# Kernel optimization log

Hardware: AMD Instinct MI355X
Metric: run time of the kernel (lower is better)

## Reference

```python
import jax, jax.numpy as jnp
import numpy as np

NUM_EXPERTS = 8
HIDDEN = 1024
INTER = 1024
BATCH = 2
SEQ = 1024
TOP_K = 2
SWIGLU_ALPHA = 1.702
LIMIT = 7.0


def setup_inputs() -> dict:
    key = jax.random.key(0)
    ks = jax.random.split(key, 7)
    hidden_states = jax.random.normal(ks[0], (BATCH, SEQ, HIDDEN), jnp.float32)
    router_indices = jax.random.randint(ks[1], (BATCH * SEQ, TOP_K), 0, NUM_EXPERTS)
    routing_weights = jax.nn.softmax(
        jax.random.normal(ks[2], (BATCH * SEQ, NUM_EXPERTS), jnp.float32), axis=-1)
    scale = 0.02
    gate_up_proj = jax.random.normal(ks[3], (NUM_EXPERTS, HIDDEN, 2 * INTER), jnp.float32) * scale
    gate_up_proj_bias = jax.random.normal(ks[4], (NUM_EXPERTS, 2 * INTER), jnp.float32) * scale
    down_proj = jax.random.normal(ks[5], (NUM_EXPERTS, INTER, HIDDEN), jnp.float32) * scale
    down_proj_bias = jax.random.normal(ks[6], (NUM_EXPERTS, HIDDEN), jnp.float32) * scale
    return {
        "hidden_states": hidden_states,
        "router_indices": router_indices,
        "routing_weights": routing_weights,
        "gate_up_proj": gate_up_proj,
        "gate_up_proj_bias": gate_up_proj_bias,
        "down_proj": down_proj,
        "down_proj_bias": down_proj_bias,
    }


def _grouped_mm(x, w, expert_ids):
    """Grouped GEMM: y[t] = x[t] @ w[expert_ids[t]].

    x: [T, K], w: [E, K, N], expert_ids: [T] int.
    Reference form via one-hot masking (exact equivalent of torch._grouped_mm
    on expert-sorted tokens); guaranteed jit- and grad-safe.
    """
    onehot = jax.nn.one_hot(expert_ids, w.shape[0], dtype=x.dtype)  # [T, E]
    y_all = jnp.einsum('tk,ekn->etn', x, w)                         # [E, T, N]
    return jnp.einsum('te,etn->tn', onehot, y_all)                  # [T, N]


def _gpt_oss_swiglu(x):
    gate = jnp.minimum(x[..., ::2], LIMIT)
    up = jnp.clip(x[..., 1::2], -LIMIT, LIMIT)
    glu = gate * jax.nn.sigmoid(gate * SWIGLU_ALPHA)
    return (up + 1.0) * glu


def reference(hidden_states, router_indices, routing_weights,
              gate_up_proj, gate_up_proj_bias, down_proj, down_proj_bias):
    B = hidden_states.shape[0]
    H = hidden_states.shape[-1]
    x = hidden_states.reshape(-1, H)                       # [M, H]
    M = x.shape[0]
    top_k = router_indices.shape[1]
    num_experts = gate_up_proj.shape[0]

    # routing_weights is [M, num_experts] -> gather the top-k weights
    topk_weights = jnp.take_along_axis(routing_weights, router_indices, axis=1)  # [M, K]

    flat_experts = router_indices.reshape(-1)              # [T = M*K]
    sort_idx = jnp.argsort(flat_experts)                   # expert-sorted order
    sorted_pos = sort_idx // top_k                         # token id per slot
    expert_sorted = flat_experts[sort_idx]                 # [T]
    grouped = x[sorted_pos]                                # [T, H]

    gate_up = _grouped_mm(grouped, gate_up_proj, expert_sorted)
    gate_up = gate_up + gate_up_proj_bias[expert_sorted]   # per-expert bias
    inter = _gpt_oss_swiglu(gate_up)                       # [T, I]

    down = _grouped_mm(inter, down_proj, expert_sorted)
    down = down + down_proj_bias[expert_sorted]            # [T, H]
    down = down * topk_weights.reshape(-1)[sort_idx][:, None]

    out = jnp.zeros((M, H), x.dtype).at[sorted_pos].add(down)  # scatter-add combine
    return out.reshape(B, -1, H)
```

## Files before the change

kernel.cpp:

```cpp
#include <hip/hip_runtime.h>

#define NE 8
#define NH 1024
#define NI 1024
#define NGU 2048
#define MTOK 2048
#define TSLOT 4096

#define MAXT64 80
#define MAXT128 40

typedef short s16x8 __attribute__((ext_vector_type(8)));
typedef float f32x4 __attribute__((ext_vector_type(4)));
typedef unsigned short u16;

#define WS_SEG      0
#define WS_DESC64   64
#define WS_DESC128  384
#define WS_SLOT     1024
#define WS_POS      17408
#define WS_INTER    33792
#define WS_AREG     8422400UL
#define WS_WREG     12616704UL
#define WS_WTD      46171136UL
#define WS_NEED_FAST  46171136UL
#define WS_NEED_PIGGY 62948352UL

__device__ inline u16 f2bf(float f) {
    unsigned u = __builtin_bit_cast(unsigned, f);
    u += 0x7fffu + ((u >> 16) & 1u);
    return (u16)(u >> 16);
}

__device__ inline void lds_dma16(const u16* g, u16* l) {
    __builtin_amdgcn_global_load_lds(
        (const __attribute__((address_space(1))) unsigned int*)g,
        (__attribute__((address_space(3))) unsigned int*)l, 16, 0, 0);
}

__device__ inline int lds_off(int row, int blk) {
    return (row << 7) | (((blk ^ (row & 7)) & 7) << 4);
}

#define PIPE_FENCE asm volatile("" ::: "memory")
#define WAIT_VM6   asm volatile("s_waitcnt vmcnt(6)" ::: "memory")
#define WAIT_VM0   asm volatile("s_waitcnt vmcnt(0)" ::: "memory")

__device__ inline void tr_tile(const float* __restrict__ in, u16* __restrict__ outw,
                               int K, int N, int n0, int k0, int tid, u16 (*T)[66]) {
#pragma unroll
    for (int p = 0; p < 2; ++p) {
        int kr = p * 32 + (tid >> 4) * 2;
        int nc = (tid & 15) * 4;
        const float* r0 = in + (size_t)(k0 + kr) * N + n0 + nc;
        float4 v0 = *(const float4*)r0;
        float4 v1 = *(const float4*)(r0 + N);
#pragma unroll
        for (int i = 0; i < 4; ++i) {
            unsigned lo = f2bf(((const float*)&v0)[i]);
            unsigned hi = f2bf(((const float*)&v1)[i]);
            *(unsigned*)&T[nc + i][kr] = lo | (hi << 16);
        }
    }
    __syncthreads();
#pragma unroll
    for (int p = 0; p < 2; ++p) {
        int idx = p * 256 + tid;
        int nr = idx >> 3, kc = (idx & 7) * 8;
        unsigned q0 = *(const unsigned*)&T[nr][kc + 0];
        unsigned q1 = *(const unsigned*)&T[nr][kc + 2];
        unsigned q2 = *(const unsigned*)&T[nr][kc + 4];
        unsigned q3 = *(const unsigned*)&T[nr][kc + 6];
        uint4 vv = {q0, q1, q2, q3};
        *(uint4*)(outw + (size_t)(n0 + nr) * K + k0 + kc) = vv;
    }
}

__device__ inline void build_body(const int* __restrict__ ridx, int* __restrict__ seg,
                                  int* __restrict__ d64, int* __restrict__ d128,
                                  int* __restrict__ slot_of, int* __restrict__ pos_of,
                                  int* cnt, int* cur, int tid) {
    if (tid < NE) cnt[tid] = 0;
    __syncthreads();
    for (int s = tid; s < TSLOT; s += 256) atomicAdd(&cnt[ridx[s] & 7], 1);
    __syncthreads();
    if (tid == 0) {
        int a = 0;
        for (int e = 0; e < NE; ++e) { seg[e] = a; cur[e] = a; a += cnt[e]; }
        seg[NE] = a;
        int nt = 0;
        for (int e = 0; e < NE; ++e)
            for (int m0 = 0; m0 < cnt[e]; m0 += 64) d64[nt++] = (e << 16) | (m0 / 64);
        for (; nt < MAXT64; ++nt) d64[nt] = -1;
        nt = 0;
        for (int e = 0; e < NE; ++e)
            for (int m0 = 0; m0 < cnt[e]; m0 += 128) d128[nt++] = (e << 16) | (m0 / 128);
        for (; nt < MAXT128; ++nt) d128[nt] = -1;
    }
    __syncthreads();
    for (int s = tid; s < TSLOT; s += 256) {
        int e = ridx[s] & 7;
        int p = atomicAdd(&cur[e], 1);
        slot_of[p] = s;
        pos_of[s] = p;
    }
}

__device__ __forceinline__ void gemm_pipe(const u16* const ap[4], const u16* const bp[2],
                                          char* SM, int tid, int kbeg, int nsteps,
                                          f32x4 (&acc)[4][2]) {
    u16* As0 = (u16*)SM;
    u16* As1 = (u16*)(SM + 16384);
    u16* Bs0 = (u16*)(SM + 32768);
    u16* Bs1 = (u16*)(SM + 40960);
    int lane = tid & 63, w = tid >> 6;
    int ml = lane & 15, kq = lane >> 4;
    int wm = w >> 1, wn = w & 1;

    auto stage = [&](u16* AS, u16* BS, int kb) {
#pragma unroll
        for (int c = 0; c < 4; ++c) lds_dma16(ap[c] + kb, AS + c * 2048 + w * 512);
#pragma unroll
        for (int c = 0; c < 2; ++c) lds_dma16(bp[c] + kb, BS + c * 2048 + w * 512);
    };
    auto compute = [&](const u16* AS, const u16* BS) {
#pragma unroll
        for (int kk = 0; kk < 64; kk += 32) {
            s16x8 af[4], bf[2];
#pragma unroll
            for (int i = 0; i < 4; ++i)
                af[i] = *(const s16x8*)((const char*)AS + lds_off(wm * 64 + i * 16 + ml, (kk >> 3) + kq));
#pragma unroll
            for (int i = 0; i < 2; ++i)
                bf[i] = *(const s16x8*)((const char*)BS + lds_off(wn * 32 + i * 16 + ml, (kk >> 3) + kq));
#pragma unroll
            for (int mi = 0; mi < 4; ++mi)
#pragma unroll
                for (int ni = 0; ni < 2; ++ni)
                    acc[mi][ni] = __builtin_amdgcn_mfma_f32_16x16x32_bf16(
                        af[mi], bf[ni], acc[mi][ni], 0, 0, 0);
        }
    };

    stage(As0, Bs0, kbeg);
    for (int t = 0; t < nsteps; t += 2) {
        stage(As1, Bs1, kbeg + ((t + 1) << 6));
        WAIT_VM6;
        __builtin_amdgcn_s_barrier();
        PIPE_FENCE;
        __builtin_amdgcn_s_setprio(1);
        compute(As0, Bs0);
        __builtin_amdgcn_s_setprio(0);
        PIPE_FENCE;
        __builtin_amdgcn_s_barrier();
        if (t < nsteps - 2) {
            stage(As0, Bs0, kbeg + ((t + 2) << 6));
            WAIT_VM6;
        } else {
            WAIT_VM0;
        }
        __builtin_amdgcn_s_barrier();
        PIPE_FENCE;
        __builtin_amdgcn_s_setprio(1);
        compute(As1, Bs1);
        __builtin_amdgcn_s_setprio(0);
        PIPE_FENCE;
        __builtin_amdgcn_s_barrier();
    }
}

__device__ __forceinline__ void job_gateup(
        int d, int y, const u16* __restrict__ A, const u16* __restrict__ wt,
        const float* __restrict__ bias, const int* __restrict__ seg,
        const int* __restrict__ slot_of, u16* __restrict__ inter,
        char* SM, int tid) {
    int e = d >> 16, mt = d & 0xffff;
    int seg0 = seg[e], Te = seg[e + 1] - seg0, m0 = mt * 128;
    int lane = tid & 63, w = tid >> 6;
    int ml = lane & 15, kq = lane >> 4;
    int wm = w >> 1, wn = w & 1;
    int n0 = y * 64;
    int dr = lane >> 3, db = (lane & 7) ^ dr;
    const u16* wte = wt + (size_t)e * NGU * NH;

    const u16* ap[4];
#pragma unroll
    for (int c = 0; c < 4; ++c) {
        int gr = seg0 + m0 + c * 32 + w * 8 + dr;
        if (gr > TSLOT - 1) gr = TSLOT - 1;
        int tok = slot_of[gr] >> 1;
        ap[c] = A + (size_t)tok * NH + db * 8;
    }
    const u16* bp[2];
#pragma unroll
    for (int c = 0; c < 2; ++c)
        bp[c] = wte + (size_t)(n0 + c * 32 + w * 8 + dr) * NH + db * 8;

    f32x4 zero = {0.f, 0.f, 0.f, 0.f};
    f32x4 acc[4][2];
#pragma unroll
    for (int i = 0; i < 4; ++i) { acc[i][0] = zero; acc[i][1] = zero; }

    gemm_pipe(ap, bp, SM, tid, 0, 16, acc);

#pragma unroll
    for (int ni = 0; ni < 2; ++ni) {
        int n = n0 + wn * 32 + ni * 16 + ml;
        float bv = bias[e * NGU + n];
#pragma unroll
        for (int mi = 0; mi < 4; ++mi) {
#pragma unroll
            for (int r = 0; r < 4; ++r) {
                float v = acc[mi][ni][r] + bv;
                float pr = __shfl_xor(v, 1, 64);
                float g = (lane & 1) ? pr : v;
                float u = (lane & 1) ? v : pr;
                g = fminf(g, 7.0f);
                u = fminf(fmaxf(u, -7.0f), 7.0f);
                float glu = g / (1.0f + __expf(-1.702f * g));
                float yv = (u + 1.0f) * glu;
                int mloc = wm * 64 + mi * 16 + kq * 4 + r;
                if (!(lane & 1) && (m0 + mloc) < Te)
                    inter[(size_t)(seg0 + m0 + mloc) * NI + (n >> 1)] = f2bf(yv);
            }
        }
    }
}

__device__ __forceinline__ void job_down(
        int d, int y, int kz, const u16* __restrict__ inter, const u16* __restrict__ wt,
        const float* __restrict__ bias, const float* __restrict__ rw,
        const int* __restrict__ seg, const int* __restrict__ slot_of,
        float* __restrict__ out, char* SM, int tid) {
    int e = d >> 16, mt = d & 0xffff;
    int seg0 = seg[e], Te = seg[e + 1] - seg0, m0 = mt * 128;
    int* tokS = (int*)(SM + 49152);
    float* wgtS = (float*)(SM + 49664);

    if (tid < 128) {
        int m = m0 + tid;
        if (m < Te) {
            int token = slot_of[seg0 + m] >> 1;
            tokS[tid] = token;
            wgtS[tid] = rw[token * NE + e];
        } else {
            tokS[tid] = 0;
            wgtS[tid] = 0.0f;
        }
    }

    int lane = tid & 63, w = tid >> 6;
    int ml = lane & 15, kq = lane >> 4;
    int wm = w >> 1, wn = w & 1;
    int n0 = y * 64;
    int dr = lane >> 3, db = (lane & 7) ^ dr;
    const u16* wte = wt + (size_t)e * NH * NI;

    const u16* ap[4];
#pragma unroll
    for (int c = 0; c < 4; ++c) {
        int gr = seg0 + m0 + c * 32 + w * 8 + dr;
        if (gr > TSLOT - 1) gr = TSLOT - 1;
        ap[c] = inter + (size_t)gr * NI + db * 8;
    }
    const u16* bp[2];
#pragma unroll
    for (int c = 0; c < 2; ++c)
        bp[c] = wte + (size_t)(n0 + c * 32 + w * 8 + dr) * NI + db * 8;

    f32x4 zero = {0.f, 0.f, 0.f, 0.f};
    f32x4 acc[4][2];
#pragma unroll
    for (int i = 0; i < 4; ++i) { acc[i][0] = zero; acc[i][1] = zero; }

    gemm_pipe(ap, bp, SM, tid, kz * (NI / 2), 8, acc);

    float bv[2];
#pragma unroll
    for (int ni = 0; ni < 2; ++ni)
        bv[ni] = kz ? 0.0f : bias[e * NH + n0 + wn * 32 + ni * 16 + ml];

#pragma unroll
    for (int mi = 0; mi < 4; ++mi) {
#pragma unroll
        for (int r = 0; r < 4; ++r) {
            int mloc = wm * 64 + mi * 16 + kq * 4 + r;
            if ((m0 + mloc) < Te) {
                int token = tokS[mloc];
                float wgt = wgtS[mloc];
#pragma unroll
                for (int ni = 0; ni < 2; ++ni) {
                    int n = n0 + wn * 32 + ni * 16 + ml;
                    atomicAdd(&out[(size_t)token * NH + n], (acc[mi][ni][r] + bv[ni]) * wgt);
                }
            }
        }
    }
}

__global__ __launch_bounds__(256) void k_prep(
        const float* __restrict__ x, const int* __restrict__ ridx,
        const float* __restrict__ wgu, const float* __restrict__ wd,
        int* __restrict__ seg, int* __restrict__ d64, int* __restrict__ d128,
        int* __restrict__ slot_of, int* __restrict__ pos_of,
        u16* __restrict__ A, u16* __restrict__ wt_gu, u16* __restrict__ wt_d,
        float* __restrict__ out) {
    __shared__ int cnt[NE];
    __shared__ int cur[NE];
    __shared__ u16 T[64][66];
    int b = blockIdx.x;
    int tid = threadIdx.x;
    if (b == 0) {
        build_body(ridx, seg, d64, d128, slot_of, pos_of, cnt, cur, tid);
    } else if (b <= MTOK) {
        int t = b - 1;
        float4 v = ((const float4*)(x + (size_t)t * NH))[tid];
        ushort4 o;
        o.x = f2bf(v.x); o.y = f2bf(v.y); o.z = f2bf(v.z); o.w = f2bf(v.w);
        ((ushort4*)(A + (size_t)t * NH))[tid] = o;
        float4 z = {0.f, 0.f, 0.f, 0.f};
        ((float4*)(out + (size_t)t * NH))[tid] = z;
    } else if (b <= MTOK + 4096) {
        int id = b - (MTOK + 1);
        int e = id >> 9, rem = id & 511;
        int kblk = rem >> 5, nblk = rem & 31;
        tr_tile(wgu + (size_t)e * NH * NGU, wt_gu + (size_t)e * NGU * NH,
                NH, NGU, nblk * 64, kblk * 64, tid, T);
    } else {
        int id = b - (MTOK + 4097);
        int e = id >> 8, rem = id & 255;
        int kblk = rem >> 4, nblk = rem & 15;
        tr_tile(wd + (size_t)e * NI * NH, wt_d + (size_t)e * NH * NI,
                NI, NH, nblk * 64, kblk * 64, tid, T);
    }
}

__global__ __launch_bounds__(256) void k_gateup_f(
        const u16* __restrict__ A, const u16* __restrict__ wt,
        const float* __restrict__ bias,
        const int* __restrict__ seg, const int* __restrict__ desc,
        const int* __restrict__ slot_of, u16* __restrict__ inter) {
    __shared__ __align__(16) char SM[50176];
    int d = desc[blockIdx.x];
    if (d < 0) return;
    job_gateup(d, blockIdx.y, A, wt, bias, seg, slot_of, inter, SM, threadIdx.x);
}

__global__ __launch_bounds__(256) void k_down_f(
        const u16* __restrict__ inter, const u16* __restrict__ wt,
        const float* __restrict__ bias, const float* __restrict__ rw,
        const int* __restrict__ seg, const int* __restrict__ desc,
        const int* __restrict__ slot_of, float* __restrict__ out) {
    __shared__ __align__(16) char SM[50176];
    int d = desc[blockIdx.x];
    if (d < 0) return;
    job_down(d, blockIdx.y, blockIdx.z, inter, wt, bias, rw, seg, slot_of, out,
             SM, threadIdx.x);
}

__global__ __launch_bounds__(256) void k_tr(const float* __restrict__ W,
                                            u16* __restrict__ WT, int K, int N) {
    __shared__ u16 T[64][66];
    tr_tile(W + (size_t)blockIdx.z * K * N, WT + (size_t)blockIdx.z * N * K,
            K, N, blockIdx.x * 64, blockIdx.y * 64, threadIdx.x, T);
}

__global__ void k_build(const int* __restrict__ ridx, int* __restrict__ seg,
                        int* __restrict__ d64, int* __restrict__ d128,
                        int* __restrict__ slot_of, int* __restrict__ pos_of) {
    __shared__ int cnt[NE];
    __shared__ int cur[NE];
    build_body(ridx, seg, d64, d128, slot_of, pos_of, cnt, cur, threadIdx.x);
}

__global__ __launch_bounds__(256) void k_gateup_s(
        const float* __restrict__ x, const float* __restrict__ w,
        const float* __restrict__ bias,
        const int* __restrict__ seg, const int* __restrict__ desc,
        const int* __restrict__ slot_of, u16* __restrict__ inter) {
    int d = desc[blockIdx.x];
    if (d < 0) return;
    int e = d >> 16, mt = d & 0xffff;
    int seg0 = seg[e], Te = seg[e + 1] - seg0, m0 = mt * 64;
    __shared__ u16 As[64 * 40];
    __shared__ int tok[64];
    int tid = threadIdx.x;
    if (tid < 64) {
        int m = m0 + tid;
        tok[tid] = (m < Te) ? (slot_of[seg0 + m] >> 1) : -1;
    }
    __syncthreads();
    int lane = tid & 63, wave = tid >> 6;
    int arow = tid >> 2, acol = (tid & 3) * 8;
    int ta = tok[arow];
    int kq = lane >> 4, ml = lane & 15;
    int nb = blockIdx.y * 128 + wave * 32;
    const float* wp = w + (size_t)e * NH * NGU;
    f32x4 zero = {0.f, 0.f, 0.f, 0.f};
    f32x4 acc[4][2];
#pragma unroll
    for (int i = 0; i < 4; ++i) { acc[i][0] = zero; acc[i][1] = zero; }
    for (int kb = 0; kb < NH; kb += 32) {
        float4 a0 = {0, 0, 0, 0}, a1 = {0, 0, 0, 0};
        if (ta >= 0) {
            const float* xp = x + (size_t)ta * NH + kb + acol;
            a0 = *(const float4*)xp; a1 = *(const float4*)(xp + 4);
        }
        s16x8 av;
        av[0] = (short)f2bf(a0.x); av[1] = (short)f2bf(a0.y);
        av[2] = (short)f2bf(a0.z); av[3] = (short)f2bf(a0.w);
        av[4] = (short)f2bf(a1.x); av[5] = (short)f2bf(a1.y);
        av[6] = (short)f2bf(a1.z); av[7] = (short)f2bf(a1.w);
        __syncthreads();
        *(s16x8*)&As[arow * 40 + acol] = av;
        __syncthreads();
        s16x8 afr[4];
#pragma unroll
        for (int msi = 0; msi < 4; ++msi)
            afr[msi] = *(const s16x8*)&As[(msi * 16 + ml) * 40 + kq * 8];
        s16x8 bfr[2];
#pragma unroll
        for (int s = 0; s < 2; ++s) {
            const float* bp = wp + (size_t)(kb + kq * 8) * NGU + nb + s * 16 + ml;
#pragma unroll
            for (int j = 0; j < 8; ++j) bfr[s][j] = (short)f2bf(bp[(size_t)j * NGU]);
        }
#pragma unroll
        for (int msi = 0; msi < 4; ++msi)
#pragma unroll
            for (int s = 0; s < 2; ++s)
                acc[msi][s] = __builtin_amdgcn_mfma_f32_16x16x32_bf16(
                    afr[msi], bfr[s], acc[msi][s], 0, 0, 0);
    }
#pragma unroll
    for (int s = 0; s < 2; ++s) {
        int n = nb + s * 16 + ml;
        float bv = bias[e * NGU + n];
#pragma unroll
        for (int msi = 0; msi < 4; ++msi) {
#pragma unroll
            for (int r = 0; r < 4; ++r) {
                float v = acc[msi][s][r] + bv;
                float pr = __shfl_xor(v, 1, 64);
                float g = (lane & 1) ? pr : v;
                float u = (lane & 1) ? v : pr;
                g = fminf(g, 7.0f);
                u = fminf(fmaxf(u, -7.0f), 7.0f);
                float glu = g / (1.0f + __expf(-1.702f * g));
                float y = (u + 1.0f) * glu;
                int mrow = m0 + msi * 16 + kq * 4 + r;
                if (!(lane & 1) && mrow < Te)
                    inter[(size_t)(seg0 + mrow) * NI + (n >> 1)] = f2bf(y);
            }
        }
    }
}

__global__ __launch_bounds__(256) void k_down_s(
        const u16* __restrict__ inter, const float* __restrict__ w,
        const float* __restrict__ bias, const float* __restrict__ rw,
        const int* __restrict__ seg, const int* __restrict__ desc,
        const int* __restrict__ slot_of, float* __restrict__ out) {
    int d = desc[blockIdx.x];
    if (d < 0) return;
    int e = d >> 16, mt = d & 0xffff;
    int seg0 = seg[e], Te = seg[e + 1] - seg0, m0 = mt * 64;
    __shared__ u16 As[64 * 40];
    int tid = threadIdx.x;
    int lane = tid & 63, wave = tid >> 6;
    int arow = tid >> 2, acol = (tid & 3) * 8;
    bool avalid = (m0 + arow) < Te;
    int kq = lane >> 4, ml = lane & 15;
    int nb = blockIdx.y * 128 + wave * 32;
    const float* wp = w + (size_t)e * NI * NH;
    f32x4 zero = {0.f, 0.f, 0.f, 0.f};
    f32x4 acc[4][2];
#pragma unroll
    for (int i = 0; i < 4; ++i) { acc[i][0] = zero; acc[i][1] = zero; }
    for (int kb = 0; kb < NI; kb += 32) {
        s16x8 av = {0, 0, 0, 0, 0, 0, 0, 0};
        if (avalid) av = *(const s16x8*)(inter + (size_t)(seg0 + m0 + arow) * NI + kb + acol);
        __syncthreads();
        *(s16x8*)&As[arow * 40 + acol] = av;
        __syncthreads();
        s16x8 afr[4];
#pragma unroll
        for (int msi = 0; msi < 4; ++msi)
            afr[msi] = *(const s16x8*)&As[(msi * 16 + ml) * 40 + kq * 8];
        s16x8 bfr[2];
#pragma unroll
        for (int s = 0; s < 2; ++s) {
            const float* bp = wp + (size_t)(kb + kq * 8) * NH + nb + s * 16 + ml;
#pragma unroll
            for (int j = 0; j < 8; ++j) bfr[s][j] = (short)f2bf(bp[(size_t)j * NH]);
        }
#pragma unroll
        for (int msi = 0; msi < 4; ++msi)
#pragma unroll
            for (int s = 0; s < 2; ++s)
                acc[msi][s] = __builtin_amdgcn_mfma_f32_16x16x32_bf16(
                    afr[msi], bfr[s], acc[msi][s], 0, 0, 0);
    }
    float bv[2];
    bv[0] = bias[e * NH + nb + ml];
    bv[1] = bias[e * NH + nb + 16 + ml];
#pragma unroll
    for (int msi = 0; msi < 4; ++msi) {
#pragma unroll
        for (int r = 0; r < 4; ++r) {
            int mrow = m0 + msi * 16 + kq * 4 + r;
            if (mrow < Te) {
                int slot = slot_of[seg0 + mrow];
                int token = slot >> 1;
                float wgt = rw[token * NE + e];
#pragma unroll
                for (int s = 0; s < 2; ++s) {
                    int n = nb + s * 16 + ml;
                    atomicAdd(&out[(size_t)token * NH + n], (acc[msi][s][r] + bv[s]) * wgt);
                }
            }
        }
    }
}

extern "C" void kernel_launch(void* const* d_in, const int* in_sizes, int n_in,
                              void* d_out, int out_size, void* d_ws, size_t ws_size,
                              hipStream_t stream) {
    const float* x   = (const float*)d_in[0];
    const int*   ri  = (const int*)d_in[1];
    const float* rw  = (const float*)d_in[2];
    const float* wgu = (const float*)d_in[3];
    const float* bgu = (const float*)d_in[4];
    const float* wd  = (const float*)d_in[5];
    const float* bd  = (const float*)d_in[6];
    float* out = (float*)d_out;

    char* ws = (char*)d_ws;
    int* seg     = (int*)(ws + WS_SEG);
    int* d64     = (int*)(ws + WS_DESC64);
    int* d128    = (int*)(ws + WS_DESC128);
    int* slot_of = (int*)(ws + WS_SLOT);
    int* pos_of  = (int*)(ws + WS_POS);
    u16* inter   = (u16*)(ws + WS_INTER);

    if (ws_size >= WS_NEED_PIGGY) {
        u16* aReg = (u16*)(ws + WS_AREG);
        u16* wReg = (u16*)(ws + WS_WREG);
        u16* wtd  = (u16*)(ws + WS_WTD);
        hipLaunchKernelGGL(k_prep, dim3(1 + MTOK + 4096 + 2048), dim3(256), 0, stream,
                           x, ri, wgu, wd, seg, d64, d128, slot_of, pos_of,
                           aReg, wReg, wtd, out);
        hipLaunchKernelGGL(k_gateup_f, dim3(MAXT128, NGU / 64), dim3(256), 0, stream,
                           aReg, wReg, bgu, seg, d128, slot_of, inter);
        hipLaunchKernelGGL(k_down_f, dim3(MAXT128, NH / 64, 2), dim3(256), 0, stream,
                           inter, wtd, bd, rw, seg, d128, slot_of, out);
    } else if (ws_size >= WS_NEED_FAST) {
        u16* aReg = (u16*)(ws + WS_AREG);
        u16* wReg = (u16*)(ws + WS_WREG);
        hipLaunchKernelGGL(k_prep, dim3(1 + MTOK + 4096), dim3(256), 0, stream,
                           x, ri, wgu, wd, seg, d64, d128, slot_of, pos_of,
                           aReg, wReg, wReg , out);
        hipLaunchKernelGGL(k_gateup_f, dim3(MAXT128, NGU / 64), dim3(256), 0, stream,
                           aReg, wReg, bgu, seg, d128, slot_of, inter);
        hipLaunchKernelGGL(k_tr, dim3(NH / 64, NI / 64, NE), dim3(256), 0, stream,
                           wd, wReg, NI, NH);
        hipLaunchKernelGGL(k_down_f, dim3(MAXT128, NH / 64, 2), dim3(256), 0, stream,
                           inter, wReg, bd, rw, seg, d128, slot_of, out);
    } else {
        hipLaunchKernelGGL(k_build, dim3(1), dim3(256), 0, stream, ri, seg, d64, d128,
                           slot_of, pos_of);
        hipMemsetAsync(out, 0, (size_t)MTOK * NH * sizeof(float), stream);
        hipLaunchKernelGGL(k_gateup_s, dim3(MAXT64, NGU / 128), dim3(256), 0, stream,
                           x, wgu, bgu, seg, d64, slot_of, inter);
        hipLaunchKernelGGL(k_down_s, dim3(MAXT64, NH / 128), dim3(256), 0, stream,
                           inter, wd, bd, rw, seg, d64, slot_of, out);
    }
}
```

Before: 225.4 us.

## Store transposed weights in K-blocked layout and make routing sort deterministic

Result: faster. 219.2 us (-2.7%).

```diff
diff --git a/kernel.cpp b/kernel.cpp
--- a/kernel.cpp
+++ b/kernel.cpp
@@ -72,21 +72,33 @@
         unsigned q2 = *(const unsigned*)&T[nr][kc + 4];
         unsigned q3 = *(const unsigned*)&T[nr][kc + 6];
         uint4 vv = {q0, q1, q2, q3};
-        *(uint4*)(outw + (size_t)(n0 + nr) * K + k0 + kc) = vv;
+        *(uint4*)(outw + ((size_t)(k0 >> 6) * N + n0 + nr) * 64 + kc) = vv;
     }
 }
 
 __device__ inline void build_body(const int* __restrict__ ridx, int* __restrict__ seg,
                                   int* __restrict__ d64, int* __restrict__ d128,
                                   int* __restrict__ slot_of, int* __restrict__ pos_of,
-                                  int* cnt, int* cur, int tid) {
-    if (tid < NE) cnt[tid] = 0;
+                                  int tid) {
+    __shared__ int hist[256][NE];
+    __shared__ int cnt[NE];
+#pragma unroll
+    for (int e = 0; e < NE; ++e) hist[tid][e] = 0;
     __syncthreads();
-    for (int s = tid; s < TSLOT; s += 256) atomicAdd(&cnt[ridx[s] & 7], 1);
+    for (int i = 0; i < 16; ++i) {
+        int e = ridx[tid * 16 + i] & 7;
+        hist[tid][e]++;
+    }
+    __syncthreads();
+    if (tid < NE) {
+        int run = 0;
+        for (int c = 0; c < 256; ++c) { int t = hist[c][tid]; hist[c][tid] = run; run += t; }
+        cnt[tid] = run;
+    }
     __syncthreads();
     if (tid == 0) {
         int a = 0;
-        for (int e = 0; e < NE; ++e) { seg[e] = a; cur[e] = a; a += cnt[e]; }
+        for (int e = 0; e < NE; ++e) { seg[e] = a; a += cnt[e]; }
         seg[NE] = a;
         int nt = 0;
         for (int e = 0; e < NE; ++e)
@@ -98,17 +110,18 @@
         for (; nt < MAXT128; ++nt) d128[nt] = -1;
     }
     __syncthreads();
-    for (int s = tid; s < TSLOT; s += 256) {
+    for (int i = 0; i < 16; ++i) {
+        int s = tid * 16 + i;
         int e = ridx[s] & 7;
-        int p = atomicAdd(&cur[e], 1);
+        int p = seg[e] + hist[tid][e]++;
         slot_of[p] = s;
         pos_of[s] = p;
     }
 }
 
 __device__ __forceinline__ void gemm_pipe(const u16* const ap[4], const u16* const bp[2],
-                                          char* SM, int tid, int kbeg, int nsteps,
-                                          f32x4 (&acc)[4][2]) {
+                                          size_t bks, char* SM, int tid, int kbeg,
+                                          int nsteps, f32x4 (&acc)[4][2]) {
     u16* As0 = (u16*)SM;
     u16* As1 = (u16*)(SM + 16384);
     u16* Bs0 = (u16*)(SM + 32768);
@@ -120,8 +133,9 @@
     auto stage = [&](u16* AS, u16* BS, int kb) {
 #pragma unroll
         for (int c = 0; c < 4; ++c) lds_dma16(ap[c] + kb, AS + c * 2048 + w * 512);
-#pragma unroll
-        for (int c = 0; c < 2; ++c) lds_dma16(bp[c] + kb, BS + c * 2048 + w * 512);
+        size_t bo = (size_t)(kb >> 6) * bks;
+#pragma unroll
+        for (int c = 0; c < 2; ++c) lds_dma16(bp[c] + bo, BS + c * 2048 + w * 512);
     };
     auto compute = [&](const u16* AS, const u16* BS) {
 #pragma unroll
@@ -194,14 +208,14 @@
     const u16* bp[2];
 #pragma unroll
     for (int c = 0; c < 2; ++c)
-        bp[c] = wte + (size_t)(n0 + c * 32 + w * 8 + dr) * NH + db * 8;
+        bp[c] = wte + (size_t)(n0 + c * 32 + w * 8 + dr) * 64 + db * 8;
 
     f32x4 zero = {0.f, 0.f, 0.f, 0.f};
     f32x4 acc[4][2];
 #pragma unroll
     for (int i = 0; i < 4; ++i) { acc[i][0] = zero; acc[i][1] = zero; }
 
-    gemm_pipe(ap, bp, SM, tid, 0, 16, acc);
+    gemm_pipe(ap, bp, (size_t)NGU * 64, SM, tid, 0, 16, acc);
 
 #pragma unroll
     for (int ni = 0; ni < 2; ++ni) {
@@ -266,14 +280,14 @@
     const u16* bp[2];
 #pragma unroll
     for (int c = 0; c < 2; ++c)
-        bp[c] = wte + (size_t)(n0 + c * 32 + w * 8 + dr) * NI + db * 8;
+        bp[c] = wte + (size_t)(n0 + c * 32 + w * 8 + dr) * 64 + db * 8;
 
     f32x4 zero = {0.f, 0.f, 0.f, 0.f};
     f32x4 acc[4][2];
 #pragma unroll
     for (int i = 0; i < 4; ++i) { acc[i][0] = zero; acc[i][1] = zero; }
 
-    gemm_pipe(ap, bp, SM, tid, kz * (NI / 2), 8, acc);
+    gemm_pipe(ap, bp, (size_t)NH * 64, SM, tid, kz * (NI / 2), 8, acc);
 
     float bv[2];
 #pragma unroll
@@ -305,13 +319,11 @@
         int* __restrict__ slot_of, int* __restrict__ pos_of,
         u16* __restrict__ A, u16* __restrict__ wt_gu, u16* __restrict__ wt_d,
         float* __restrict__ out) {
-    __shared__ int cnt[NE];
-    __shared__ int cur[NE];
     __shared__ u16 T[64][66];
     int b = blockIdx.x;
     int tid = threadIdx.x;
     if (b == 0) {
-        build_body(ridx, seg, d64, d128, slot_of, pos_of, cnt, cur, tid);
+        build_body(ridx, seg, d64, d128, slot_of, pos_of, tid);
     } else if (b <= MTOK) {
         int t = b - 1;
         float4 v = ((const float4*)(x + (size_t)t * NH))[tid];
@@ -368,9 +380,7 @@
 __global__ void k_build(const int* __restrict__ ridx, int* __restrict__ seg,
                         int* __restrict__ d64, int* __restrict__ d128,
                         int* __restrict__ slot_of, int* __restrict__ pos_of) {
-    __shared__ int cnt[NE];
-    __shared__ int cur[NE];
-    build_body(ridx, seg, d64, d128, slot_of, pos_of, cnt, cur, threadIdx.x);
+    build_body(ridx, seg, d64, d128, slot_of, pos_of, threadIdx.x);
 }
 
 __global__ __launch_bounds__(256) void k_gateup_s(
```
